# Performance work log

Hardware: AMD Instinct MI355X
Metric: run time of the kernel (lower is better)

## Reference

```python
import jax, jax.numpy as jnp
import numpy as np

B, S, D, H = 2, 2048, 1024, 16
DK = D // H


def setup_inputs() -> dict:
    key = jax.random.key(0)
    ks = jax.random.split(key, 12)
    scale = 1.0 / np.sqrt(D)
    inp = {
        "q": jax.random.normal(ks[0], (B, S, D), jnp.float32),
        "k": jax.random.normal(ks[1], (B, S, D), jnp.float32),
        "v": jax.random.normal(ks[2], (B, S, D), jnp.float32),
        # causal mask: 1 = attend, 0 = mask, broadcastable to (B, 1, S, S)
        "mask": jnp.tril(jnp.ones((S, S), jnp.int32))[None, None, :, :],
        "Wq": jax.random.normal(ks[3], (D, D), jnp.float32) * scale,
        "bq": jax.random.normal(ks[4], (D,), jnp.float32) * scale,
        "Wk": jax.random.normal(ks[5], (D, D), jnp.float32) * scale,
        "bk": jax.random.normal(ks[6], (D,), jnp.float32) * scale,
        "Wv": jax.random.normal(ks[7], (D, D), jnp.float32) * scale,
        "bv": jax.random.normal(ks[8], (D,), jnp.float32) * scale,
        "Wo": jax.random.normal(ks[9], (D, D), jnp.float32) * scale,
        "bo": jax.random.normal(ks[10], (D,), jnp.float32) * scale,
    }
    return inp


def _split_heads(x):
    b, s, _ = x.shape
    return x.reshape(b, s, H, DK).transpose(0, 2, 1, 3)  # (b, h, s, dk)


def reference(q, k, v, mask, Wq, bq, Wk, bk, Wv, bv, Wo, bo):
    Q = _split_heads(q @ Wq.T + bq)
    K = _split_heads(k @ Wk.T + bk)
    V = _split_heads(v @ Wv.T + bv)
    scores = jnp.einsum("bhqd,bhkd->bhqk", Q, K) * (DK ** -0.5)
    scores = jnp.where(mask == 0, -jnp.inf, scores)
    attn = jax.nn.softmax(scores, axis=-1)  # dropout p=0.0 -> identity
    out = jnp.einsum("bhqk,bhkd->bhqd", attn, V)
    out = out.transpose(0, 2, 1, 3).reshape(q.shape[0], q.shape[1], D)
    return out @ Wo.T + bo
```

## Files before the change

### kernel.cpp

```cpp
#include <hip/hip_runtime.h>


#define S_LEN 2048
#define NHEAD 16
#define DMODEL 1024
#define DKH 64
#define LDA 72

typedef unsigned short u16;
typedef unsigned int u32;
typedef __attribute__((ext_vector_type(8))) short short8;
typedef __attribute__((ext_vector_type(8))) __bf16 bf16x8;
typedef __attribute__((ext_vector_type(4))) float f32x4;
typedef __attribute__((ext_vector_type(16))) float f32x16;
typedef __attribute__((ext_vector_type(4))) unsigned int u32x4;

__device__ inline u16 f2bf(float f) {
  return __builtin_bit_cast(u16, (__bf16)f);
}
__device__ inline u32 pk2(float a, float b) {
  return (u32)f2bf(a) | ((u32)f2bf(b) << 16);
}

__device__ inline f32x4 mfma16x16(bf16x8 a, bf16x8 b, f32x4 c) {
  return __builtin_amdgcn_mfma_f32_16x16x32_bf16(a, b, c, 0, 0, 0);
}
__device__ inline f32x16 mfma32(bf16x8 a, bf16x8 b, f32x16 c) {
  return __builtin_amdgcn_mfma_f32_32x32x16_bf16(a, b, c, 0, 0, 0);
}

__device__ inline short8 pack8(float4 a, float4 b) {
  short8 r;
  r[0] = (short)f2bf(a.x); r[1] = (short)f2bf(a.y);
  r[2] = (short)f2bf(a.z); r[3] = (short)f2bf(a.w);
  r[4] = (short)f2bf(b.x); r[5] = (short)f2bf(b.y);
  r[6] = (short)f2bf(b.z); r[7] = (short)f2bf(b.w);
  return r;
}

typedef const __attribute__((address_space(1))) unsigned GU32;
typedef __attribute__((address_space(3))) unsigned LU32;
__device__ inline void gl2lds16(const void* g, void* l) {
  __builtin_amdgcn_global_load_lds((GU32*)g, (LU32*)l, 16, 0, 0);
}

#define SWZ(row, col8) (((row) * 8 + ((col8) ^ ((row) & 7))) * 8)

__global__ __launch_bounds__(256)
void conv_bf16(const float* __restrict__ w0, const float* __restrict__ w1,
               const float* __restrict__ w2, const float* __restrict__ w3,
               const float* __restrict__ aq, const float* __restrict__ ak,
               const float* __restrict__ av,
               u16* __restrict__ o0, u16* __restrict__ o1,
               u16* __restrict__ o2, u16* __restrict__ o3,
               u16* __restrict__ oq, u16* __restrict__ ok, u16* __restrict__ ov)
{
  const int y = blockIdx.y;
  const float* s; u16* d; int n;
  switch (y) {
    case 0: s = w0; d = o0; n = 1 << 20; break;
    case 1: s = w1; d = o1; n = 1 << 20; break;
    case 2: s = w2; d = o2; n = 1 << 20; break;
    case 3: s = w3; d = o3; n = 1 << 20; break;
    case 4: s = aq; d = oq; n = 1 << 22; break;
    case 5: s = ak; d = ok; n = 1 << 22; break;
    default: s = av; d = ov; n = 1 << 22; break;
  }
  const int i = (blockIdx.x * 256 + threadIdx.x) * 8;
  if (i >= n) return;
  float4 a = *(const float4*)&s[i];
  float4 b = *(const float4*)&s[i + 4];
  *(short8*)&d[i] = pack8(a, b);
}

__global__ __launch_bounds__(256)
void conv_w(const float* __restrict__ w0, const float* __restrict__ w1,
            const float* __restrict__ w2, const float* __restrict__ w3,
            u16* __restrict__ o0, u16* __restrict__ o1,
            u16* __restrict__ o2, u16* __restrict__ o3)
{
  const int z = blockIdx.y;
  const float* s = z == 0 ? w0 : z == 1 ? w1 : z == 2 ? w2 : w3;
  u16* d = z == 0 ? o0 : z == 1 ? o1 : z == 2 ? o2 : o3;
  const int i = (blockIdx.x * 256 + threadIdx.x) * 8;
  float4 a = *(const float4*)&s[i];
  float4 b = *(const float4*)&s[i + 4];
  *(short8*)&d[i] = pack8(a, b);
}

__global__ __launch_bounds__(256)
void proj_gemm_bf16(const u16* __restrict__ Aqb, const u16* __restrict__ Akb,
                    const u16* __restrict__ Avb,
                    const u16* __restrict__ Bq, const u16* __restrict__ Bk,
                    const u16* __restrict__ Bv,
                    const float* __restrict__ cq, const float* __restrict__ ck,
                    const float* __restrict__ cv,
                    u16* __restrict__ Oq, u16* __restrict__ Ok, u16* __restrict__ Ov)
{
  __shared__ u16 SM[4 * 8192];

  const int hw = blockIdx.x + (blockIdx.y << 3) + (blockIdx.z << 8);
  const int xcd = hw & 7, sq = hw >> 3;
  const int pan = sq % 12, xb = sq / 12;
  const int p = pan * 8 + xcd;
  const int zz = p >> 5, py = p & 31;

  const u16* Ab = zz == 0 ? Aqb : zz == 1 ? Akb : Avb;
  const u16* Wb = zz == 0 ? Bq : zz == 1 ? Bk : Bv;
  const float* bias = zz == 0 ? cq : zz == 1 ? ck : cv;

  const int t = threadIdx.x;
  const int lane = t & 63;
  const int wv = t >> 6;
  const int wm = wv >> 1, wn = wv & 1;
  const int g = lane >> 4, lr = lane & 15;
  const int bm = py << 7, bn = xb << 7;
  const int K = DMODEL;

  auto STAGE = [&](int buf, int kt) {
    const int k0 = kt << 6;
    u16* Asb = SM + buf * 8192;
    u16* Bsb = SM + 16384 + buf * 8192;
#pragma unroll
    for (int i = 0; i < 4; ++i) {
      int c = t + (i << 8);
      int row = c >> 3, col8 = c & 7;
      int c8s = col8 ^ (row & 7);
      gl2lds16(&Ab[(size_t)(bm + row) * K + k0 + c8s * 8], &Asb[c * 8]);
      gl2lds16(&Wb[(size_t)(bn + row) * K + k0 + c8s * 8], &Bsb[c * 8]);
    }
  };

  f32x4 acc[4][4] = {};
  STAGE(0, 0);
  __syncthreads();
  for (int kt = 0; kt < 16; ++kt) {
    const int cur = kt & 1;
    if (kt + 1 < 16) STAGE(cur ^ 1, kt + 1);
    u16* Asb = SM + cur * 8192;
    u16* Bsb = SM + 16384 + cur * 8192;
    bf16x8 af[2][4], bf[2][4];
#pragma unroll
    for (int kc = 0; kc < 2; ++kc)
#pragma unroll
      for (int f = 0; f < 4; ++f) {
        af[kc][f] = *(const bf16x8*)&Asb[SWZ(wm * 64 + f * 16 + lr, kc * 4 + g)];
        bf[kc][f] = *(const bf16x8*)&Bsb[SWZ(wn * 64 + f * 16 + lr, kc * 4 + g)];
      }
#pragma unroll
    for (int kc = 0; kc < 2; ++kc)
#pragma unroll
      for (int fm = 0; fm < 4; ++fm)
#pragma unroll
        for (int fn = 0; fn < 4; ++fn)
          acc[fm][fn] = mfma16x16(af[kc][fm], bf[kc][fn], acc[fm][fn]);
    __syncthreads();
  }

  if (zz == 2) {
    u16* TL = SM;
    const int b = bm >> 11, s0 = bm & (S_LEN - 1), h0 = bn >> 6;
#pragma unroll
    for (int hh = 0; hh < 2; ++hh) {
      __syncthreads();
      if (wn == hh) {
#pragma unroll
        for (int fm = 0; fm < 4; ++fm)
#pragma unroll
          for (int fn = 0; fn < 4; ++fn) {
            const int lch = fn * 16 + lr;
            const float bb = bias[bn + hh * 64 + lch];
#pragma unroll
            for (int r = 0; r < 4; ++r)
              TL[lch * 132 + wm * 64 + fm * 16 + g * 4 + r] = f2bf(acc[fm][fn][r] + bb);
          }
      }
      __syncthreads();
#pragma unroll
      for (int i = 0; i < 4; ++i) {
        int c = t + (i << 8);
        int dk = c >> 4, sc = (c & 15) << 3;
        short8 vv = *(const short8*)&TL[dk * 132 + sc];
        *(short8*)&Ov[(((size_t)(b * NHEAD + h0 + hh)) * DKH + dk) * S_LEN + s0 + sc] = vv;
      }
    }
  } else {
    u16* Out = zz == 0 ? Oq : Ok;
#pragma unroll
    for (int fm = 0; fm < 4; ++fm)
#pragma unroll
      for (int fn = 0; fn < 4; ++fn) {
        const int col = bn + wn * 64 + fn * 16 + lr;
        const int h = col >> 6, dk = col & (DKH - 1);
        const float bb = bias[col];
#pragma unroll
        for (int r = 0; r < 4; ++r) {
          const int row = bm + wm * 64 + fm * 16 + g * 4 + r;
          const int b = row >> 11, s = row & (S_LEN - 1);
          Out[(((size_t)(b * NHEAD + h)) * S_LEN + s) * DKH + dk] = f2bf(acc[fm][fn][r] + bb);
        }
      }
  }
}

__global__ __launch_bounds__(256)
void proj_gemm_f32(const float* __restrict__ Aq, const float* __restrict__ Akk,
                   const float* __restrict__ Av,
                   const u16* __restrict__ Bq, const u16* __restrict__ Bk,
                   const u16* __restrict__ Bv,
                   const float* __restrict__ cq, const float* __restrict__ ck,
                   const float* __restrict__ cv,
                   u16* __restrict__ Oq, u16* __restrict__ Ok, u16* __restrict__ Ov)
{
  __shared__ u16 SM[3 * 8192];
  u16* As = SM;
  u16* Bs0 = SM + 8192;
  u16* Bs1 = SM + 16384;

  const int hw = blockIdx.x + (blockIdx.y << 3) + (blockIdx.z << 8);
  const int xcd = hw & 7, sq = hw >> 3;
  const int pan = sq % 12, xb = sq / 12;
  const int p = pan * 8 + xcd;
  const int zz = p >> 5, py = p & 31;

  const float* Af = zz == 0 ? Aq : zz == 1 ? Akk : Av;
  const u16* Wb = zz == 0 ? Bq : zz == 1 ? Bk : Bv;
  const float* bias = zz == 0 ? cq : zz == 1 ? ck : cv;

  const int t = threadIdx.x;
  const int lane = t & 63;
  const int wv = t >> 6;
  const int wm = wv >> 1, wn = wv & 1;
  const int g = lane >> 4, lr = lane & 15;
  const int bm = py << 7, bn = xb << 7;
  const int K = DMODEL;

  float4 ax[4], ay[4];
  auto ALOAD = [&](int kt) {
    const int k0 = kt << 6;
#pragma unroll
    for (int i = 0; i < 4; ++i) {
      int c = t + (i << 8);
      int row = c >> 3, col8 = c & 7;
      const float* src = &Af[(size_t)(bm + row) * K + k0 + col8 * 8];
      ax[i] = *(const float4*)src;
      ay[i] = *(const float4*)(src + 4);
    }
  };
  auto AWRITE = [&]() {
#pragma unroll
    for (int i = 0; i < 4; ++i) {
      int c = t + (i << 8);
      int row = c >> 3, col8 = c & 7;
      *(short8*)&As[SWZ(row, col8)] = pack8(ax[i], ay[i]);
    }
  };
  auto BSTAGE = [&](u16* buf, int kt) {
    const int k0 = kt << 6;
#pragma unroll
    for (int i = 0; i < 4; ++i) {
      int c = t + (i << 8);
      int row = c >> 3, col8 = c & 7;
      int c8s = col8 ^ (row & 7);
      gl2lds16(&Wb[(size_t)(bn + row) * K + k0 + c8s * 8], &buf[c * 8]);
    }
  };

  f32x4 acc[4][4] = {};
  ALOAD(0);
  BSTAGE(Bs0, 0);
  AWRITE();
  __syncthreads();
  for (int kt = 0; kt < 16; ++kt) {
    u16* Bcur = (kt & 1) ? Bs1 : Bs0;
    u16* Bnxt = (kt & 1) ? Bs0 : Bs1;
    const bool more = (kt + 1 < 16);
    if (more) { ALOAD(kt + 1); BSTAGE(Bnxt, kt + 1); }
    bf16x8 af[2][4], bf[2][4];
#pragma unroll
    for (int kc = 0; kc < 2; ++kc)
#pragma unroll
      for (int f = 0; f < 4; ++f) {
        af[kc][f] = *(const bf16x8*)&As[SWZ(wm * 64 + f * 16 + lr, kc * 4 + g)];
        bf[kc][f] = *(const bf16x8*)&Bcur[SWZ(wn * 64 + f * 16 + lr, kc * 4 + g)];
      }
#pragma unroll
    for (int kc = 0; kc < 2; ++kc)
#pragma unroll
      for (int fm = 0; fm < 4; ++fm)
#pragma unroll
        for (int fn = 0; fn < 4; ++fn)
          acc[fm][fn] = mfma16x16(af[kc][fm], bf[kc][fn], acc[fm][fn]);
    __syncthreads();
    if (more) {
      AWRITE();
      __syncthreads();
    }
  }

  if (zz == 2) {
    u16* TL = SM;
    const int b = bm >> 11, s0 = bm & (S_LEN - 1), h0 = bn >> 6;
#pragma unroll
    for (int hh = 0; hh < 2; ++hh) {
      __syncthreads();
      if (wn == hh) {
#pragma unroll
        for (int fm = 0; fm < 4; ++fm)
#pragma unroll
          for (int fn = 0; fn < 4; ++fn) {
            const int lch = fn * 16 + lr;
            const float bb = bias[bn + hh * 64 + lch];
#pragma unroll
            for (int r = 0; r < 4; ++r)
              TL[lch * 132 + wm * 64 + fm * 16 + g * 4 + r] = f2bf(acc[fm][fn][r] + bb);
          }
      }
      __syncthreads();
#pragma unroll
      for (int i = 0; i < 4; ++i) {
        int c = t + (i << 8);
        int dk = c >> 4, sc = (c & 15) << 3;
        short8 vv = *(const short8*)&TL[dk * 132 + sc];
        *(short8*)&Ov[(((size_t)(b * NHEAD + h0 + hh)) * DKH + dk) * S_LEN + s0 + sc] = vv;
      }
    }
  } else {
    u16* Out = zz == 0 ? Oq : Ok;
#pragma unroll
    for (int fm = 0; fm < 4; ++fm)
#pragma unroll
      for (int fn = 0; fn < 4; ++fn) {
        const int col = bn + wn * 64 + fn * 16 + lr;
        const int h = col >> 6, dk = col & (DKH - 1);
        const float bb = bias[col];
#pragma unroll
        for (int r = 0; r < 4; ++r) {
          const int row = bm + wm * 64 + fm * 16 + g * 4 + r;
          const int b = row >> 11, s = row & (S_LEN - 1);
          Out[(((size_t)(b * NHEAD + h)) * S_LEN + s) * DKH + dk] = f2bf(acc[fm][fn][r] + bb);
        }
      }
  }
}

__global__ __launch_bounds__(256)
void out_gemm(const u16* __restrict__ Ao, const u16* __restrict__ Wb,
              const float* __restrict__ bias, float* __restrict__ Out)
{
  __shared__ u16 SM[4 * 8192];
  const int hw = blockIdx.x + (blockIdx.y << 3);
  const int xcd = hw & 7, sq = hw >> 3;
  const int pan = sq & 3, xb = sq >> 2;
  const int prow = pan * 8 + xcd;

  const int t = threadIdx.x;
  const int lane = t & 63;
  const int wv = t >> 6;
  const int wm = wv >> 1, wn = wv & 1;
  const int g = lane >> 4, lr = lane & 15;
  const int bm = prow << 7, bn = xb << 7;
  const int K = DMODEL;

  auto STAGE = [&](int buf, int kt) {
    const int k0 = kt << 6;
    u16* Asb = SM + buf * 8192;
    u16* Bsb = SM + 16384 + buf * 8192;
#pragma unroll
    for (int i = 0; i < 4; ++i) {
      int c = t + (i << 8);
      int row = c >> 3, col8 = c & 7;
      int c8s = col8 ^ (row & 7);
      int grow = bm + row;
      int b = grow >> 11, s = grow & (S_LEN - 1);
      int k = k0 + c8s * 8;
      int h = k >> 6, dk = k & (DKH - 1);
      gl2lds16(&Ao[(((size_t)(b * NHEAD + h)) * S_LEN + s) * DKH + dk], &Asb[c * 8]);
      gl2lds16(&Wb[(size_t)(bn + row) * K + k0 + c8s * 8], &Bsb[c * 8]);
    }
  };

  f32x4 acc[4][4] = {};
  STAGE(0, 0);
  __syncthreads();
  for (int kt = 0; kt < 16; ++kt) {
    const int cur = kt & 1;
    if (kt + 1 < 16) STAGE(cur ^ 1, kt + 1);
    u16* Asb = SM + cur * 8192;
    u16* Bsb = SM + 16384 + cur * 8192;
    bf16x8 af[2][4], bf[2][4];
#pragma unroll
    for (int kc = 0; kc < 2; ++kc)
#pragma unroll
      for (int f = 0; f < 4; ++f) {
        af[kc][f] = *(const bf16x8*)&Asb[SWZ(wm * 64 + f * 16 + lr, kc * 4 + g)];
        bf[kc][f] = *(const bf16x8*)&Bsb[SWZ(wn * 64 + f * 16 + lr, kc * 4 + g)];
      }
#pragma unroll
    for (int kc = 0; kc < 2; ++kc)
#pragma unroll
      for (int fm = 0; fm < 4; ++fm)
#pragma unroll
        for (int fn = 0; fn < 4; ++fn)
          acc[fm][fn] = mfma16x16(af[kc][fm], bf[kc][fn], acc[fm][fn]);
    __syncthreads();
  }
#pragma unroll
  for (int fm = 0; fm < 4; ++fm)
#pragma unroll
    for (int fn = 0; fn < 4; ++fn) {
      const int col = bn + wn * 64 + fn * 16 + lr;
      const float bb = bias[col];
#pragma unroll
      for (int r = 0; r < 4; ++r) {
        const int row = bm + wm * 64 + fm * 16 + g * 4 + r;
        Out[(size_t)row * DMODEL + col] = acc[fm][fn][r] + bb;
      }
    }
}

__global__ __launch_bounds__(256)
void attn_fwd(const u16* __restrict__ Qh, const u16* __restrict__ Kh,
              const u16* __restrict__ Vtg, u16* __restrict__ Ao)
{
  __shared__ u16 Ks[2][64 * LDA];
  __shared__ u16 Vs[2][64 * LDA];
  const int t = threadIdx.x, lane = t & 63, w = t >> 6;
  const int l31 = lane & 31, hi = lane >> 5;
  const int bh = blockIdx.y;
  const int pA = blockIdx.x;
  const int tA = pA, tB = 31 - pA;
  const int tT = (w < 2) ? tA : tB;
  const int qg = tT * 64 + (w & 1) * 32 + l31;
  const u16* Qb = Qh + (size_t)bh * S_LEN * DKH;
  const u16* Kb = Kh + (size_t)bh * S_LEN * DKH;
  const u16* Vb = Vtg + (size_t)bh * DKH * S_LEN;

  bf16x8 qf[4];
#pragma unroll
  for (int ks = 0; ks < 4; ++ks)
    qf[ks] = *(const bf16x8*)&Qb[(size_t)qg * DKH + ks * 16 + 8 * hi];

  f32x16 o0 = {}, o1 = {};
  float m = -1e30f, l = 0.f;

  const int r0 = t >> 3;
  const int c0 = (t & 7) << 3;
  short8 kr0, kr1, vr0, vr1;

  auto LOADT = [&](int kt) {
    const int kv0 = kt << 6;
    kr0 = *(const short8*)&Kb[(size_t)(kv0 + r0) * DKH + c0];
    kr1 = *(const short8*)&Kb[(size_t)(kv0 + r0 + 32) * DKH + c0];
    vr0 = *(const short8*)&Vb[(size_t)r0 * S_LEN + kv0 + c0];
    vr1 = *(const short8*)&Vb[(size_t)(r0 + 32) * S_LEN + kv0 + c0];
  };
  auto WRITET = [&](int b) {
    *(short8*)&Ks[b][r0 * LDA + c0] = kr0;
    *(short8*)&Ks[b][(r0 + 32) * LDA + c0] = kr1;
    *(short8*)&Vs[b][r0 * LDA + c0] = vr0;
    *(short8*)&Vs[b][(r0 + 32) * LDA + c0] = vr1;
  };

  const float C2 = 0.18033688011f;
  const int nt = tB + 1;
  LOADT(0);
  WRITET(0);
  for (int kt = 0; kt < nt; ++kt) {
    const int cur = kt & 1;
    const bool more = (kt + 1 < nt);
    if (more) LOADT(kt + 1);
    __syncthreads();
    if (w >= 2 || kt <= tA) {
      f32x16 s0 = {}, s1 = {};
#pragma unroll
      for (int ks = 0; ks < 4; ++ks) {
        bf16x8 k0 = *(const bf16x8*)&Ks[cur][(l31) * LDA + ks * 16 + 8 * hi];
        bf16x8 k1 = *(const bf16x8*)&Ks[cur][(32 + l31) * LDA + ks * 16 + 8 * hi];
        s0 = mfma32(k0, qf[ks], s0);
        s1 = mfma32(k1, qf[ks], s1);
      }
      if (kt == tT) {
        const int kv0 = kt << 6;
#pragma unroll
        for (int r = 0; r < 16; ++r) {
          const int cr = (r & 3) + 8 * (r >> 2) + 4 * hi;
          if (kv0 + cr > qg) s0[r] = -1e30f;
          if (kv0 + 32 + cr > qg) s1[r] = -1e30f;
        }
      }
      float pm = fmaxf(s0[0], s0[1]);
#pragma unroll
      for (int r = 2; r < 16; ++r) pm = fmaxf(pm, s0[r]);
#pragma unroll
      for (int r = 0; r < 16; ++r) pm = fmaxf(pm, s1[r]);
      pm = fmaxf(pm, __shfl_xor(pm, 32, 64));
      float alpha = 1.0f;
      if (!__all(pm - m <= 64.0f)) {
        const float mn = fmaxf(m, pm);
        alpha = exp2f((m - mn) * C2);
        m = mn;
#pragma unroll
        for (int r = 0; r < 16; ++r) { o0[r] *= alpha; o1[r] *= alpha; }
      }
      const float mC = m * C2;
      float rs = 0.f;
#pragma unroll
      for (int r = 0; r < 16; ++r) {
        s0[r] = exp2f(fmaf(s0[r], C2, -mC));
        s1[r] = exp2f(fmaf(s1[r], C2, -mC));
        rs += s0[r] + s1[r];
      }
      rs += __shfl_xor(rs, 32, 64);
      l = l * alpha + rs;
      bf16x8 pb[4];
#pragma unroll
      for (int s = 0; s < 4; ++s) {
        const int rb = (s & 1) * 8;
        float e0, e1, e2, e3, e4, e5, e6, e7;
        if (s >> 1) {
          e0 = s1[rb+0]; e1 = s1[rb+1]; e2 = s1[rb+2]; e3 = s1[rb+3];
          e4 = s1[rb+4]; e5 = s1[rb+5]; e6 = s1[rb+6]; e7 = s1[rb+7];
        } else {
          e0 = s0[rb+0]; e1 = s0[rb+1]; e2 = s0[rb+2]; e3 = s0[rb+3];
          e4 = s0[rb+4]; e5 = s0[rb+5]; e6 = s0[rb+6]; e7 = s0[rb+7];
        }
        u32 wlo  = pk2(e0, e1);
        u32 wlo2 = pk2(e2, e3);
        u32 whi  = pk2(e4, e5);
        u32 whi2 = pk2(e6, e7);
        u32 sA = __shfl_xor(wlo, 32, 64);
        u32 sB = __shfl_xor(wlo2, 32, 64);
        u32 sC = __shfl_xor(whi, 32, 64);
        u32 sD = __shfl_xor(whi2, 32, 64);
        u32x4 uw;
        uw[0] = hi ? sC : wlo;
        uw[1] = hi ? sD : wlo2;
        uw[2] = hi ? whi : sA;
        uw[3] = hi ? whi2 : sB;
        pb[s] = __builtin_bit_cast(bf16x8, uw);
      }
#pragma unroll
      for (int s = 0; s < 4; ++s) {
        bf16x8 v0 = *(const bf16x8*)&Vs[cur][(l31) * LDA + s * 16 + 8 * hi];
        bf16x8 v1 = *(const bf16x8*)&Vs[cur][(32 + l31) * LDA + s * 16 + 8 * hi];
        o0 = mfma32(v0, pb[s], o0);
        o1 = mfma32(v1, pb[s], o1);
      }
    }
    if (more) WRITET(cur ^ 1);
  }

  const float il = __builtin_amdgcn_rcpf(l);
  __syncthreads();
  u16* Os = (w < 2) ? Ks[0] : Ks[1];
  const int rl = (w & 1) * 32 + l31;
#pragma unroll
  for (int r = 0; r < 16; ++r) {
    const int cr = (r & 3) + 8 * (r >> 2) + 4 * hi;
    Os[rl * LDA + cr] = f2bf(o0[r] * il);
    Os[rl * LDA + 32 + cr] = f2bf(o1[r] * il);
  }
  __syncthreads();
#pragma unroll
  for (int i = 0; i < 2; ++i) {
    const int rr = r0 + i * 32;
    *(short8*)&Ao[((size_t)bh * S_LEN + tA * 64 + rr) * DKH + c0] =
        *(const short8*)&Ks[0][rr * LDA + c0];
    *(short8*)&Ao[((size_t)bh * S_LEN + tB * 64 + rr) * DKH + c0] =
        *(const short8*)&Ks[1][rr * LDA + c0];
  }
}

extern "C" void kernel_launch(void* const* d_in, const int* in_sizes, int n_in,
                              void* d_out, int out_size, void* d_ws, size_t ws_size,
                              hipStream_t stream)
{
  (void)in_sizes; (void)n_in; (void)out_size;
  const float* q  = (const float*)d_in[0];
  const float* k  = (const float*)d_in[1];
  const float* v  = (const float*)d_in[2];
  const float* Wq = (const float*)d_in[4];
  const float* bq = (const float*)d_in[5];
  const float* Wk = (const float*)d_in[6];
  const float* bk = (const float*)d_in[7];
  const float* Wv = (const float*)d_in[8];
  const float* bv = (const float*)d_in[9];
  const float* Wo = (const float*)d_in[10];
  const float* bo = (const float*)d_in[11];

  char* ws = (char*)d_ws;
  const size_t MB = 1024 * 1024;

  if (ws_size >= 56 * MB) {
    u16* Wqb = (u16*)(ws);
    u16* Wkb = (u16*)(ws + 2 * MB);
    u16* Wvb = (u16*)(ws + 4 * MB);
    u16* Wob = (u16*)(ws + 6 * MB);
    u16* qb  = (u16*)(ws + 8 * MB);
    u16* kb  = (u16*)(ws + 16 * MB);
    u16* vb  = (u16*)(ws + 24 * MB);
    u16* Qh  = (u16*)(ws + 32 * MB);
    u16* Kh  = (u16*)(ws + 40 * MB);
    u16* Vt  = (u16*)(ws + 48 * MB);
    u16* Ao  = qb;

    conv_bf16<<<dim3(2048, 7), 256, 0, stream>>>(Wq, Wk, Wv, Wo, q, k, v,
                                                 Wqb, Wkb, Wvb, Wob, qb, kb, vb);
    proj_gemm_bf16<<<dim3(8, 32, 3), 256, 0, stream>>>(qb, kb, vb, Wqb, Wkb, Wvb,
                                                       bq, bk, bv, Qh, Kh, Vt);
    attn_fwd<<<dim3(16, 2 * NHEAD), 256, 0, stream>>>(Qh, Kh, Vt, Ao);
    out_gemm<<<dim3(8, 32), 256, 0, stream>>>(Ao, Wob, bo, (float*)d_out);
  } else {
    u16* Wqb = (u16*)(ws);
    u16* Wkb = (u16*)(ws + 2 * MB);
    u16* Wvb = (u16*)(ws + 4 * MB);
    u16* Wob = (u16*)(ws + 6 * MB);
    u16* Qh  = (u16*)(ws + 8 * MB);
    u16* Kh  = (u16*)(ws + 16 * MB);
    u16* Vt  = (u16*)(ws + 24 * MB);
    u16* Ao  = (u16*)(ws + 32 * MB);

    conv_w<<<dim3(512, 4), 256, 0, stream>>>(Wq, Wk, Wv, Wo, Wqb, Wkb, Wvb, Wob);
    proj_gemm_f32<<<dim3(8, 32, 3), 256, 0, stream>>>(q, k, v, Wqb, Wkb, Wvb,
                                                      bq, bk, bv, Qh, Kh, Vt);
    attn_fwd<<<dim3(16, 2 * NHEAD), 256, 0, stream>>>(Qh, Kh, Vt, Ao);
    out_gemm<<<dim3(8, 32), 256, 0, stream>>>(Ao, Wob, bo, (float*)d_out);
  }
}
```

Before: 145.9 us.

## Process four query tiles per attention block to share K/V staging

Each attention block now handles four 64-row query tiles (two balanced causal pairs) instead of two, with each wave owning two 32-row query groups and two independent online-softmax states. One K/V tile staged in LDS serves twice as many queries, halving global K/V traffic, and the grid shrinks from 16 to 8 blocks per head. The trade-off is higher register pressure (launch bounds now allow one block per SIMD), fewer blocks in flight (256 total on a 256-CU part), and less latency hiding.

Result: slower. 149.2 us (+2.3%).

```diff
diff --git a/kernel.cpp b/kernel.cpp
--- a/kernel.cpp
+++ b/kernel.cpp
@@ -419,30 +419,33 @@
     }
 }
 
-__global__ __launch_bounds__(256)
+__global__ __launch_bounds__(256, 1)
 void attn_fwd(const u16* __restrict__ Qh, const u16* __restrict__ Kh,
               const u16* __restrict__ Vtg, u16* __restrict__ Ao)
 {
-  __shared__ u16 Ks[2][64 * LDA];
-  __shared__ u16 Vs[2][64 * LDA];
+  __shared__ u16 SM2[4][64 * LDA];
   const int t = threadIdx.x, lane = t & 63, w = t >> 6;
   const int l31 = lane & 31, hi = lane >> 5;
   const int bh = blockIdx.y;
-  const int pA = blockIdx.x;
-  const int tA = pA, tB = 31 - pA;
-  const int tT = (w < 2) ? tA : tB;
-  const int qg = tT * 64 + (w & 1) * 32 + l31;
+  const int p = blockIdx.x;
+  const int grp = w >> 1, cg = w & 1;
+  const int tTA = p + grp * 8;
+  const int tTB = 31 - grp * 8 - p;
+  const int qgA = tTA * 64 + cg * 32 + l31;
+  const int qgB = tTB * 64 + cg * 32 + l31;
   const u16* Qb = Qh + (size_t)bh * S_LEN * DKH;
   const u16* Kb = Kh + (size_t)bh * S_LEN * DKH;
   const u16* Vb = Vtg + (size_t)bh * DKH * S_LEN;
 
-  bf16x8 qf[4];
-#pragma unroll
-  for (int ks = 0; ks < 4; ++ks)
-    qf[ks] = *(const bf16x8*)&Qb[(size_t)qg * DKH + ks * 16 + 8 * hi];
-
-  f32x16 o0 = {}, o1 = {};
-  float m = -1e30f, l = 0.f;
+  bf16x8 qfA[4], qfB[4];
+#pragma unroll
+  for (int ks = 0; ks < 4; ++ks) {
+    qfA[ks] = *(const bf16x8*)&Qb[(size_t)qgA * DKH + ks * 16 + 8 * hi];
+    qfB[ks] = *(const bf16x8*)&Qb[(size_t)qgB * DKH + ks * 16 + 8 * hi];
+  }
+
+  f32x16 oA0 = {}, oA1 = {}, oB0 = {}, oB1 = {};
+  float mA = -1e30f, lA = 0.f, mB = -1e30f, lB = 0.f;
 
   const int r0 = t >> 3;
   const int c0 = (t & 7) << 3;
@@ -456,14 +459,96 @@
     vr1 = *(const short8*)&Vb[(size_t)(r0 + 32) * S_LEN + kv0 + c0];
   };
   auto WRITET = [&](int b) {
-    *(short8*)&Ks[b][r0 * LDA + c0] = kr0;
-    *(short8*)&Ks[b][(r0 + 32) * LDA + c0] = kr1;
-    *(short8*)&Vs[b][r0 * LDA + c0] = vr0;
-    *(short8*)&Vs[b][(r0 + 32) * LDA + c0] = vr1;
+    *(short8*)&SM2[b][r0 * LDA + c0] = kr0;
+    *(short8*)&SM2[b][(r0 + 32) * LDA + c0] = kr1;
+    *(short8*)&SM2[2 + b][r0 * LDA + c0] = vr0;
+    *(short8*)&SM2[2 + b][(r0 + 32) * LDA + c0] = vr1;
   };
 
   const float C2 = 0.18033688011f;
-  const int nt = tB + 1;
+
+  auto C32 = [&](int cur, const bf16x8* qf, f32x16& o0, f32x16& o1,
+                 float& m, float& l, bool diag, int qg, int kt) {
+    const u16* Kl = &SM2[cur][0];
+    const u16* Vl = &SM2[2 + cur][0];
+    f32x16 s0 = {}, s1 = {};
+#pragma unroll
+    for (int ks = 0; ks < 4; ++ks) {
+      bf16x8 k0 = *(const bf16x8*)&Kl[(l31) * LDA + ks * 16 + 8 * hi];
+      bf16x8 k1 = *(const bf16x8*)&Kl[(32 + l31) * LDA + ks * 16 + 8 * hi];
+      s0 = mfma32(k0, qf[ks], s0);
+      s1 = mfma32(k1, qf[ks], s1);
+    }
+    if (diag) {
+      const int kv0 = kt << 6;
+#pragma unroll
+      for (int r = 0; r < 16; ++r) {
+        const int cr = (r & 3) + 8 * (r >> 2) + 4 * hi;
+        if (kv0 + cr > qg) s0[r] = -1e30f;
+        if (kv0 + 32 + cr > qg) s1[r] = -1e30f;
+      }
+    }
+    float pm = fmaxf(s0[0], s0[1]);
+#pragma unroll
+    for (int r = 2; r < 16; ++r) pm = fmaxf(pm, s0[r]);
+#pragma unroll
+    for (int r = 0; r < 16; ++r) pm = fmaxf(pm, s1[r]);
+    pm = fmaxf(pm, __shfl_xor(pm, 32, 64));
+    float alpha = 1.0f;
+    if (!__all(pm - m <= 64.0f)) {
+      const float mn = fmaxf(m, pm);
+      alpha = exp2f((m - mn) * C2);
+      m = mn;
+#pragma unroll
+      for (int r = 0; r < 16; ++r) { o0[r] *= alpha; o1[r] *= alpha; }
+    }
+    const float mC = m * C2;
+    float rs = 0.f;
+#pragma unroll
+    for (int r = 0; r < 16; ++r) {
+      s0[r] = exp2f(fmaf(s0[r], C2, -mC));
+      s1[r] = exp2f(fmaf(s1[r], C2, -mC));
+      rs += s0[r] + s1[r];
+    }
+    rs += __shfl_xor(rs, 32, 64);
+    l = l * alpha + rs;
+    bf16x8 pb[4];
+#pragma unroll
+    for (int s = 0; s < 4; ++s) {
+      const int rb = (s & 1) * 8;
+      float e0, e1, e2, e3, e4, e5, e6, e7;
+      if (s >> 1) {
+        e0 = s1[rb+0]; e1 = s1[rb+1]; e2 = s1[rb+2]; e3 = s1[rb+3];
+        e4 = s1[rb+4]; e5 = s1[rb+5]; e6 = s1[rb+6]; e7 = s1[rb+7];
+      } else {
+        e0 = s0[rb+0]; e1 = s0[rb+1]; e2 = s0[rb+2]; e3 = s0[rb+3];
+        e4 = s0[rb+4]; e5 = s0[rb+5]; e6 = s0[rb+6]; e7 = s0[rb+7];
+      }
+      u32 wlo  = pk2(e0, e1);
+      u32 wlo2 = pk2(e2, e3);
+      u32 whi  = pk2(e4, e5);
+      u32 whi2 = pk2(e6, e7);
+      u32 sA = __shfl_xor(wlo, 32, 64);
+      u32 sB = __shfl_xor(wlo2, 32, 64);
+      u32 sC = __shfl_xor(whi, 32, 64);
+      u32 sD = __shfl_xor(whi2, 32, 64);
+      u32x4 uw;
+      uw[0] = hi ? sC : wlo;
+      uw[1] = hi ? sD : wlo2;
+      uw[2] = hi ? whi : sA;
+      uw[3] = hi ? whi2 : sB;
+      pb[s] = __builtin_bit_cast(bf16x8, uw);
+    }
+#pragma unroll
+    for (int s = 0; s < 4; ++s) {
+      bf16x8 v0 = *(const bf16x8*)&Vl[(l31) * LDA + s * 16 + 8 * hi];
+      bf16x8 v1 = *(const bf16x8*)&Vl[(32 + l31) * LDA + s * 16 + 8 * hi];
+      o0 = mfma32(v0, pb[s], o0);
+      o1 = mfma32(v1, pb[s], o1);
+    }
+  };
+
+  const int nt = 32 - p;
   LOADT(0);
   WRITET(0);
   for (int kt = 0; kt < nt; ++kt) {
@@ -471,104 +556,36 @@
     const bool more = (kt + 1 < nt);
     if (more) LOADT(kt + 1);
     __syncthreads();
-    if (w >= 2 || kt <= tA) {
-      f32x16 s0 = {}, s1 = {};
-#pragma unroll
-      for (int ks = 0; ks < 4; ++ks) {
-        bf16x8 k0 = *(const bf16x8*)&Ks[cur][(l31) * LDA + ks * 16 + 8 * hi];
-        bf16x8 k1 = *(const bf16x8*)&Ks[cur][(32 + l31) * LDA + ks * 16 + 8 * hi];
-        s0 = mfma32(k0, qf[ks], s0);
-        s1 = mfma32(k1, qf[ks], s1);
-      }
-      if (kt == tT) {
-        const int kv0 = kt << 6;
-#pragma unroll
-        for (int r = 0; r < 16; ++r) {
-          const int cr = (r & 3) + 8 * (r >> 2) + 4 * hi;
-          if (kv0 + cr > qg) s0[r] = -1e30f;
-          if (kv0 + 32 + cr > qg) s1[r] = -1e30f;
-        }
-      }
-      float pm = fmaxf(s0[0], s0[1]);
-#pragma unroll
-      for (int r = 2; r < 16; ++r) pm = fmaxf(pm, s0[r]);
-#pragma unroll
-      for (int r = 0; r < 16; ++r) pm = fmaxf(pm, s1[r]);
-      pm = fmaxf(pm, __shfl_xor(pm, 32, 64));
-      float alpha = 1.0f;
-      if (!__all(pm - m <= 64.0f)) {
-        const float mn = fmaxf(m, pm);
-        alpha = exp2f((m - mn) * C2);
-        m = mn;
-#pragma unroll
-        for (int r = 0; r < 16; ++r) { o0[r] *= alpha; o1[r] *= alpha; }
-      }
-      const float mC = m * C2;
-      float rs = 0.f;
-#pragma unroll
-      for (int r = 0; r < 16; ++r) {
-        s0[r] = exp2f(fmaf(s0[r], C2, -mC));
-        s1[r] = exp2f(fmaf(s1[r], C2, -mC));
-        rs += s0[r] + s1[r];
-      }
-      rs += __shfl_xor(rs, 32, 64);
-      l = l * alpha + rs;
-      bf16x8 pb[4];
-#pragma unroll
-      for (int s = 0; s < 4; ++s) {
-        const int rb = (s & 1) * 8;
-        float e0, e1, e2, e3, e4, e5, e6, e7;
-        if (s >> 1) {
-          e0 = s1[rb+0]; e1 = s1[rb+1]; e2 = s1[rb+2]; e3 = s1[rb+3];
-          e4 = s1[rb+4]; e5 = s1[rb+5]; e6 = s1[rb+6]; e7 = s1[rb+7];
-        } else {
-          e0 = s0[rb+0]; e1 = s0[rb+1]; e2 = s0[rb+2]; e3 = s0[rb+3];
-          e4 = s0[rb+4]; e5 = s0[rb+5]; e6 = s0[rb+6]; e7 = s0[rb+7];
-        }
-        u32 wlo  = pk2(e0, e1);
-        u32 wlo2 = pk2(e2, e3);
-        u32 whi  = pk2(e4, e5);
-        u32 whi2 = pk2(e6, e7);
-        u32 sA = __shfl_xor(wlo, 32, 64);
-        u32 sB = __shfl_xor(wlo2, 32, 64);
-        u32 sC = __shfl_xor(whi, 32, 64);
-        u32 sD = __shfl_xor(whi2, 32, 64);
-        u32x4 uw;
-        uw[0] = hi ? sC : wlo;
-        uw[1] = hi ? sD : wlo2;
-        uw[2] = hi ? whi : sA;
-        uw[3] = hi ? whi2 : sB;
-        pb[s] = __builtin_bit_cast(bf16x8, uw);
-      }
-#pragma unroll
-      for (int s = 0; s < 4; ++s) {
-        bf16x8 v0 = *(const bf16x8*)&Vs[cur][(l31) * LDA + s * 16 + 8 * hi];
-        bf16x8 v1 = *(const bf16x8*)&Vs[cur][(32 + l31) * LDA + s * 16 + 8 * hi];
-        o0 = mfma32(v0, pb[s], o0);
-        o1 = mfma32(v1, pb[s], o1);
-      }
-    }
+    if (kt <= tTA) C32(cur, qfA, oA0, oA1, mA, lA, kt == tTA, qgA, kt);
+    if (kt <= tTB) C32(cur, qfB, oB0, oB1, mB, lB, kt == tTB, qgB, kt);
     if (more) WRITET(cur ^ 1);
   }
 
-  const float il = __builtin_amdgcn_rcpf(l);
+  const float ilA = __builtin_amdgcn_rcpf(lA);
+  const float ilB = __builtin_amdgcn_rcpf(lB);
   __syncthreads();
-  u16* Os = (w < 2) ? Ks[0] : Ks[1];
-  const int rl = (w & 1) * 32 + l31;
+  u16* OsA = &SM2[0][0] + (size_t)grp * 64 * LDA;
+  u16* OsB = &SM2[0][0] + (size_t)(2 + grp) * 64 * LDA;
+  const int rl = cg * 32 + l31;
 #pragma unroll
   for (int r = 0; r < 16; ++r) {
     const int cr = (r & 3) + 8 * (r >> 2) + 4 * hi;
-    Os[rl * LDA + cr] = f2bf(o0[r] * il);
-    Os[rl * LDA + 32 + cr] = f2bf(o1[r] * il);
+    OsA[rl * LDA + cr] = f2bf(oA0[r] * ilA);
+    OsA[rl * LDA + 32 + cr] = f2bf(oA1[r] * ilA);
+    OsB[rl * LDA + cr] = f2bf(oB0[r] * ilB);
+    OsB[rl * LDA + 32 + cr] = f2bf(oB1[r] * ilB);
   }
   __syncthreads();
 #pragma unroll
-  for (int i = 0; i < 2; ++i) {
-    const int rr = r0 + i * 32;
-    *(short8*)&Ao[((size_t)bh * S_LEN + tA * 64 + rr) * DKH + c0] =
-        *(const short8*)&Ks[0][rr * LDA + c0];
-    *(short8*)&Ao[((size_t)bh * S_LEN + tB * 64 + rr) * DKH + c0] =
-        *(const short8*)&Ks[1][rr * LDA + c0];
+  for (int i = 0; i < 8; ++i) {
+    const int c = t + (i << 8);
+    const int tile = c >> 9;
+    const int row = (c >> 3) & 63;
+    const int c8 = (c & 7) << 3;
+    const int tq = (tile == 0) ? p : (tile == 1) ? p + 8
+                 : (tile == 2) ? 31 - p : 23 - p;
+    *(short8*)&Ao[((size_t)bh * S_LEN + tq * 64 + row) * DKH + c8] =
+        *(const short8*)(&SM2[0][0] + (size_t)tile * 64 * LDA + row * LDA + c8);
   }
 }
 
@@ -609,7 +626,7 @@
                                                  Wqb, Wkb, Wvb, Wob, qb, kb, vb);
     proj_gemm_bf16<<<dim3(8, 32, 3), 256, 0, stream>>>(qb, kb, vb, Wqb, Wkb, Wvb,
                                                        bq, bk, bv, Qh, Kh, Vt);
-    attn_fwd<<<dim3(16, 2 * NHEAD), 256, 0, stream>>>(Qh, Kh, Vt, Ao);
+    attn_fwd<<<dim3(8, 2 * NHEAD), 256, 0, stream>>>(Qh, Kh, Vt, Ao);
     out_gemm<<<dim3(8, 32), 256, 0, stream>>>(Ao, Wob, bo, (float*)d_out);
   } else {
     u16* Wqb = (u16*)(ws);
@@ -624,7 +641,7 @@
     conv_w<<<dim3(512, 4), 256, 0, stream>>>(Wq, Wk, Wv, Wo, Wqb, Wkb, Wvb, Wob);
     proj_gemm_f32<<<dim3(8, 32, 3), 256, 0, stream>>>(q, k, v, Wqb, Wkb, Wvb,
                                                       bq, bk, bv, Qh, Kh, Vt);
-    attn_fwd<<<dim3(16, 2 * NHEAD), 256, 0, stream>>>(Qh, Kh, Vt, Ao);
+    attn_fwd<<<dim3(8, 2 * NHEAD), 256, 0, stream>>>(Qh, Kh, Vt, Ao);
     out_gemm<<<dim3(8, 32), 256, 0, stream>>>(Ao, Wob, bo, (float*)d_out);
   }
 }
```
